# Kernel tuning notes

Measured on AMD Instinct MI355X. Metric: run time of the kernel, lower is better.

Reference implementation:

```python
import jax, jax.numpy as jnp
import numpy as np

N = 50000      # nodes
E = 400000     # edges
IN = 64        # in_channels
HID = 64       # hidden_channels
H = 4          # num_heads
LAT = 32       # latent_dim
NEG_SLOPE = 0.2


def setup_inputs() -> dict:
    key = jax.random.key(0)
    ks = jax.random.split(key, 20)
    w = lambda k, shape, s=0.05: (jax.random.normal(k, shape, jnp.float32) * s)
    inp = {
        'x': jax.random.normal(ks[0], (N, IN), jnp.float32),
        'edge_index': jax.random.randint(ks[1], (2, E), 0, N, dtype=jnp.int32),
        'batch': jnp.zeros((N,), jnp.int32),
        'eps': jax.random.normal(ks[2], (N, LAT), jnp.float32),
        # conv1: in -> HID per head, 4 heads, concat
        'W1': w(ks[3], (IN, H * HID)), 'a_src1': w(ks[4], (H, HID)), 'a_dst1': w(ks[5], (H, HID)), 'b1': jnp.zeros((H * HID,), jnp.float32),
        # conv2: H*HID -> HID per head, concat
        'W2': w(ks[6], (H * HID, H * HID)), 'a_src2': w(ks[7], (H, HID)), 'a_dst2': w(ks[8], (H, HID)), 'b2': jnp.zeros((H * HID,), jnp.float32),
        # conv_mu / conv_logvar: H*HID -> LAT, 1 head, no concat
        'Wmu': w(ks[9], (H * HID, LAT)), 'a_src_mu': w(ks[10], (1, LAT)), 'a_dst_mu': w(ks[11], (1, LAT)), 'b_mu': jnp.zeros((LAT,), jnp.float32),
        'Wlv': w(ks[12], (H * HID, LAT)), 'a_src_lv': w(ks[13], (1, LAT)), 'a_dst_lv': w(ks[14], (1, LAT)), 'b_lv': jnp.zeros((LAT,), jnp.float32),
        # decoder
        'W_fc': w(ks[15], (LAT, HID)), 'b_fc': jnp.zeros((HID,), jnp.float32),
        'W_node': w(ks[16], (HID, IN)), 'b_node': jnp.zeros((IN,), jnp.float32),
        'W_edge': w(ks[17], (HID, 1)), 'b_edge': jnp.zeros((1,), jnp.float32),
    }
    return inp


def gat_layer(x, W, a_src, a_dst, b, src, dst, concat):
    """PyG-style GATConv: gather -> leaky_relu score -> per-dst softmax -> scatter-add."""
    n = x.shape[0]
    heads, c = a_src.shape
    h = (x @ W).reshape(n, heads, c)                     # [N,H,C]
    s_src = jnp.einsum('nhc,hc->nh', h, a_src)           # [N,H]
    s_dst = jnp.einsum('nhc,hc->nh', h, a_dst)
    e = jax.nn.leaky_relu(s_src[src] + s_dst[dst], NEG_SLOPE)   # [E,H]
    m = jax.ops.segment_max(e, dst, num_segments=n)      # stable softmax per destination
    e = jnp.exp(e - m[dst])
    denom = jax.ops.segment_sum(e, dst, num_segments=n)
    alpha = e / (denom[dst] + 1e-16)                     # [E,H]
    out = jax.ops.segment_sum(alpha[:, :, None] * h[src], dst, num_segments=n)  # [N,H,C]
    out = out.reshape(n, heads * c) if concat else out.mean(axis=1)
    return out + b


def reference(x, edge_index, batch, eps,
              W1, a_src1, a_dst1, b1,
              W2, a_src2, a_dst2, b2,
              Wmu, a_src_mu, a_dst_mu, b_mu,
              Wlv, a_src_lv, a_dst_lv, b_lv,
              W_fc, b_fc, W_node, b_node, W_edge, b_edge):
    n = x.shape[0]
    src0, dst0 = edge_index[0], edge_index[1]
    loops = jnp.arange(n, dtype=edge_index.dtype)        # GATConv add_self_loops=True
    src = jnp.concatenate([src0, loops])
    dst = jnp.concatenate([dst0, loops])

    # encode
    h = jax.nn.relu(gat_layer(x, W1, a_src1, a_dst1, b1, src, dst, concat=True))
    h = jax.nn.relu(gat_layer(h, W2, a_src2, a_dst2, b2, src, dst, concat=True))
    mu = gat_layer(h, Wmu, a_src_mu, a_dst_mu, b_mu, src, dst, concat=False)
    logvar = gat_layer(h, Wlv, a_src_lv, a_dst_lv, b_lv, src, dst, concat=False)

    # reparameterize (eps supplied for determinism)
    z = mu + eps * jnp.exp(0.5 * logvar)

    # decode
    zd = jax.nn.relu(z @ W_fc + b_fc)                    # [N,HID]
    node_features = zd @ W_node + b_node                 # [N,IN]
    edge_feat = zd[src0] * zd[dst0]                      # [E,HID]
    edge_scores = (edge_feat @ W_edge + b_edge).squeeze(-1)  # [E]
    return (mu, logvar, z, node_features, edge_scores)
```

## Files before the change

kernel.cpp:

```cpp
#include <hip/hip_runtime.h>
#include <math.h>

#define NEG_SLOPE 0.2f

__device__ __forceinline__ float lky(float x){ return x > 0.f ? x : NEG_SLOPE * x; }

__device__ __forceinline__ unsigned short f2bf(float f){
  unsigned int u = __float_as_uint(f);
  unsigned int r = (u + 0x7fffu + ((u >> 16) & 1u)) >> 16;
  return (unsigned short)r;
}
__device__ __forceinline__ float bf2f(unsigned short s){
  return __uint_as_float(((unsigned int)s) << 16);
}
__device__ __forceinline__ void unp8(uint4 v, float* f){
  f[0]=__uint_as_float(v.x<<16); f[1]=__uint_as_float(v.x&0xffff0000u);
  f[2]=__uint_as_float(v.y<<16); f[3]=__uint_as_float(v.y&0xffff0000u);
  f[4]=__uint_as_float(v.z<<16); f[5]=__uint_as_float(v.z&0xffff0000u);
  f[6]=__uint_as_float(v.w<<16); f[7]=__uint_as_float(v.w&0xffff0000u);
}
__device__ __forceinline__ uint4 pack8(const float* o){
  uint4 v;
  v.x = (unsigned)f2bf(o[0]) | ((unsigned)f2bf(o[1])<<16);
  v.y = (unsigned)f2bf(o[2]) | ((unsigned)f2bf(o[3])<<16);
  v.z = (unsigned)f2bf(o[4]) | ((unsigned)f2bf(o[5])<<16);
  v.w = (unsigned)f2bf(o[6]) | ((unsigned)f2bf(o[7])<<16);
  return v;
}

typedef __bf16 bf16x8 __attribute__((ext_vector_type(8)));
typedef float  f32x4  __attribute__((ext_vector_type(4)));
typedef float  f32x2  __attribute__((ext_vector_type(2)));

__device__ __forceinline__ uint2 pk_fp8(const float* f){
  unsigned lo = 0u, hi = 0u;
  lo = __builtin_amdgcn_cvt_pk_fp8_f32(f[0], f[1], (int)lo, false);
  lo = __builtin_amdgcn_cvt_pk_fp8_f32(f[2], f[3], (int)lo, true);
  hi = __builtin_amdgcn_cvt_pk_fp8_f32(f[4], f[5], (int)hi, false);
  hi = __builtin_amdgcn_cvt_pk_fp8_f32(f[6], f[7], (int)hi, true);
  return make_uint2(lo, hi);
}
__device__ __forceinline__ void unpk_fp8(uint2 v, float* f){
  f32x2 a0 = __builtin_amdgcn_cvt_pk_f32_fp8((int)v.x, false);
  f32x2 a1 = __builtin_amdgcn_cvt_pk_f32_fp8((int)v.x, true);
  f32x2 a2 = __builtin_amdgcn_cvt_pk_f32_fp8((int)v.y, false);
  f32x2 a3 = __builtin_amdgcn_cvt_pk_f32_fp8((int)v.y, true);
  f[0]=a0[0]; f[1]=a0[1]; f[2]=a1[0]; f[3]=a1[1];
  f[4]=a2[0]; f[5]=a2[1]; f[6]=a3[0]; f[7]=a3[1];
}

__global__ void zero_ints_kernel(int* __restrict__ p, int n){
  int i = blockIdx.x * blockDim.x + threadIdx.x;
  if (i < n) p[i] = 0;
}
__global__ void count_deg_kernel(const int* __restrict__ dst, int* __restrict__ deg, int E){
  int e = blockIdx.x * blockDim.x + threadIdx.x;
  if (e < E) atomicAdd(&deg[dst[e]], 1);
}
__global__ void scan_chunk_kernel(const int* __restrict__ deg, int* __restrict__ rowptr,
                                  int* __restrict__ bsum, int n){
  __shared__ int s[256];
  int t = threadIdx.x;
  int i = blockIdx.x * 256 + t;
  int v = (i < n) ? deg[i] : 0;
  s[t] = v; __syncthreads();
  for (int off = 1; off < 256; off <<= 1){
    int x = (t >= off) ? s[t - off] : 0;
    __syncthreads();
    s[t] += x;
    __syncthreads();
  }
  if (i < n) rowptr[i + 1] = s[t];
  if (t == 255) bsum[blockIdx.x] = s[255];
}
__global__ void scan_bsum_kernel(const int* __restrict__ bsum, int* __restrict__ boff, int nb){
  __shared__ int s[256];
  int t = threadIdx.x;
  int v = (t < nb) ? bsum[t] : 0;
  s[t] = v; __syncthreads();
  for (int off = 1; off < 256; off <<= 1){
    int x = (t >= off) ? s[t - off] : 0;
    __syncthreads();
    s[t] += x;
    __syncthreads();
  }
  boff[t] = s[t] - v;
}
__global__ void scan_add_kernel(int* __restrict__ rowptr, const int* __restrict__ boff, int n){
  int i = blockIdx.x * 256 + threadIdx.x;
  if (i < n) rowptr[i + 1] += boff[blockIdx.x];
  if (i == 0) rowptr[0] = 0;
}
__global__ void fill_csr_kernel(const int* __restrict__ src, const int* __restrict__ dst,
                                const int* __restrict__ rowptr, int* __restrict__ cursor,
                                int* __restrict__ colv, int E){
  int e = blockIdx.x * blockDim.x + threadIdx.x;
  if (e >= E) return;
  int d = dst[e];
  int pos = atomicAdd(&cursor[d], 1);
  colv[rowptr[d] + pos] = src[e];
}

__global__ void pack_w_kernel(const float* __restrict__ Wa, const float* __restrict__ Wb,
                              int K, int M, int Mhalf, unsigned short* __restrict__ out){
  int idx = blockIdx.x * 256 + threadIdx.x;
  if (idx >= K * M) return;
  int j = idx & 7;
  int l = (idx >> 3) & 63;
  int rest = idx >> 9;
  int KS = K >> 5;
  int s = rest % KS, gct = rest / KS;
  int col = gct * 16 + (l & 15);
  int k   = s * 32 + ((l >> 4) << 3) + j;
  float v;
  if (Wb == nullptr) v = Wa[(long)k * M + col];
  else v = (col < Mhalf) ? Wa[(long)k * Mhalf + col] : Wb[(long)k * Mhalf + (col - Mhalf)];
  out[idx] = f2bf(v);
}

__global__ void make_p1_kernel(const float* __restrict__ W1, const float* __restrict__ as1,
                               const float* __restrict__ ad1, float* __restrict__ P1){
  int idx = blockIdx.x * 256 + threadIdx.x;
  if (idx >= 512) return;
  int sd = idx & 1, h = (idx >> 1) & 3, k = idx >> 3;
  const float* av = sd ? ad1 : as1;
  float acc = 0.f;
  for (int c = 0; c < 64; ++c) acc += W1[k * 256 + h * 64 + c] * av[h * 64 + c];
  P1[idx] = acc;
}

__global__ __launch_bounds__(256) void score1cvt_kernel(
    const float* __restrict__ x, const float* __restrict__ P1,
    unsigned short* __restrict__ xb,
    float* __restrict__ S1s, float* __restrict__ S1d, int n)
{
  __shared__ float P[512];
  int t = threadIdx.x;
  P[t] = P1[t]; P[t + 256] = P1[t + 256];
  __syncthreads();
  int nid = blockIdx.x * 256 + t;
  if (nid >= n) return;
  const float4* xr = (const float4*)x + (long)nid * 16;
  uint4* xw = (uint4*)xb + (long)nid * 8;
  float acc[8] = {0,0,0,0,0,0,0,0};
  for (int kc = 0; kc < 16; kc += 2){
    float4 v0 = xr[kc], v1 = xr[kc + 1];
    uint4 o;
    o.x = (unsigned)f2bf(v0.x) | ((unsigned)f2bf(v0.y) << 16);
    o.y = (unsigned)f2bf(v0.z) | ((unsigned)f2bf(v0.w) << 16);
    o.z = (unsigned)f2bf(v1.x) | ((unsigned)f2bf(v1.y) << 16);
    o.w = (unsigned)f2bf(v1.z) | ((unsigned)f2bf(v1.w) << 16);
    xw[kc >> 1] = o;
    float vf[8] = {v0.x, v0.y, v0.z, v0.w, v1.x, v1.y, v1.z, v1.w};
    #pragma unroll
    for (int j = 0; j < 8; ++j){
      int k = kc * 4 + j;
      #pragma unroll
      for (int o8 = 0; o8 < 8; ++o8) acc[o8] += vf[j] * P[k * 8 + o8];
    }
  }
  *(float4*)(S1s + nid * 4) = make_float4(acc[0], acc[2], acc[4], acc[6]);
  *(float4*)(S1d + nid * 4) = make_float4(acc[1], acc[3], acc[5], acc[7]);
}

__global__ __launch_bounds__(256) void aggx_kernel(
    const unsigned short* __restrict__ xb,
    const float* __restrict__ Ss, const float* __restrict__ Sd,
    const int* __restrict__ rowptr, const int* __restrict__ colv,
    unsigned short* __restrict__ Xagg, int n)
{
  int wv = threadIdx.x >> 6, l = threadIdx.x & 63;
  int nid = blockIdx.x * 4 + wv;
  if (nid >= n) return;
  int slot = l >> 5;
  int cl = l & 31;
  float4 sdv = *(const float4*)(Sd + (long)nid * 4);
  float acc[4][2] = {};
  float sumw[4] = {0.f, 0.f, 0.f, 0.f};
  int beg = rowptr[nid], end = rowptr[nid + 1];
  for (int jj = beg + slot; jj < end; jj += 2){
    int s = colv[jj];
    float4 a = *(const float4*)(Ss + (long)s * 4);
    float wx = __expf(lky(a.x + sdv.x));
    float wy = __expf(lky(a.y + sdv.y));
    float wz = __expf(lky(a.z + sdv.z));
    float ww = __expf(lky(a.w + sdv.w));
    unsigned xv = *((const unsigned*)xb + (long)s * 32 + cl);
    float f0 = __uint_as_float(xv << 16);
    float f1 = __uint_as_float(xv & 0xffff0000u);
    acc[0][0] += wx * f0; acc[0][1] += wx * f1;
    acc[1][0] += wy * f0; acc[1][1] += wy * f1;
    acc[2][0] += wz * f0; acc[2][1] += wz * f1;
    acc[3][0] += ww * f0; acc[3][1] += ww * f1;
    sumw[0] += wx; sumw[1] += wy; sumw[2] += wz; sumw[3] += ww;
  }
  #pragma unroll
  for (int h = 0; h < 4; ++h){
    acc[h][0] += __shfl_xor(acc[h][0], 32);
    acc[h][1] += __shfl_xor(acc[h][1], 32);
    sumw[h]   += __shfl_xor(sumw[h], 32);
  }
  float4 ssv = *(const float4*)(Ss + (long)nid * 4);
  unsigned xv = *((const unsigned*)xb + (long)nid * 32 + cl);
  float f0 = __uint_as_float(xv << 16);
  float f1 = __uint_as_float(xv & 0xffff0000u);
  float wsh[4] = { __expf(lky(ssv.x + sdv.x)), __expf(lky(ssv.y + sdv.y)),
                   __expf(lky(ssv.z + sdv.z)), __expf(lky(ssv.w + sdv.w)) };
  if (l < 32){
    #pragma unroll
    for (int h = 0; h < 4; ++h){
      float inv = 1.f / (sumw[h] + wsh[h] + 1e-16f);
      float o0 = (acc[h][0] + wsh[h] * f0) * inv;
      float o1 = (acc[h][1] + wsh[h] * f1) * inv;
      unsigned ov = (unsigned)f2bf(o0) | ((unsigned)f2bf(o1) << 16);
      *((unsigned*)Xagg + (long)nid * 128 + h * 32 + cl) = ov;
    }
  }
}

template<int K, int KB, int CW, bool BD, bool SCORES, bool RELU, bool OUT8>
__global__ __launch_bounds__(256) void gemm_mfma_kernel(
    const unsigned short* __restrict__ Xb, const unsigned short* __restrict__ Wpk,
    const float* __restrict__ a_s, const float* __restrict__ a_d,
    const float* __restrict__ a_s2, const float* __restrict__ a_d2,
    const float* __restrict__ bias,
    void* __restrict__ Hout,
    float* __restrict__ Ss, float* __restrict__ Sd,
    float* __restrict__ Ss2, float* __restrict__ Sd2, int n)
{
  constexpr int BR  = (CW == 4) ? 32 : 128;
  constexpr int M   = 64 * CW;
  constexpr int KSB = KB / 32;
  constexpr int LDA = K + 8;
  constexpr int SH  = (BR * LDA > BR * M) ? BR * LDA : BR * M;
  __shared__ unsigned short As[SH];

  const int t = threadIdx.x;
  const int w = t >> 6, l = t & 63;
  const int quad = l >> 4, l15 = l & 15;
  const long base = (long)blockIdx.x * BR;
  const int roww = (CW == 4) ? 0 : w;
  const int colw = (CW == 4) ? w : 0;
  const int abase = BD ? w * KB : 0;

  {
    const uint4* Xg = (const uint4*)Xb;
    long g0 = base * (K / 8);
    long lim = (long)n * (K / 8);
    for (int c = t; c < BR * K / 8; c += 256){
      int row = c / (K / 8), kc = c % (K / 8);
      uint4 v = make_uint4(0u, 0u, 0u, 0u);
      if (g0 + c < lim) v = Xg[g0 + c];
      *(uint4*)(As + row * LDA + kc * 8) = v;
    }
  }
  __syncthreads();

  f32x4 acc[2][4] = {};
  for (int s = 0; s < KSB; ++s){
    bf16x8 af0 = *(const bf16x8*)(As + (roww * 32 + 0  + l15) * LDA + abase + s * 32 + quad * 8);
    bf16x8 af1 = *(const bf16x8*)(As + (roww * 32 + 16 + l15) * LDA + abase + s * 32 + quad * 8);
    #pragma unroll
    for (int ct = 0; ct < 4; ++ct){
      int gct = colw * 4 + ct;
      bf16x8 bf = *(const bf16x8*)(Wpk + (((long)gct * KSB + s) * 64 + l) * 8);
      acc[0][ct] = __builtin_amdgcn_mfma_f32_16x16x32_bf16(af0, bf, acc[0][ct], 0, 0, 0);
      acc[1][ct] = __builtin_amdgcn_mfma_f32_16x16x32_bf16(af1, bf, acc[1][ct], 0, 0, 0);
    }
  }

  if constexpr (SCORES){
    if (CW == 4){
      const int head = w;
      float asv[4], adv[4];
      #pragma unroll
      for (int ct = 0; ct < 4; ++ct){
        int col = head * 64 + ct * 16 + l15;
        asv[ct] = a_s[col]; adv[ct] = a_d[col];
      }
      #pragma unroll
      for (int rt = 0; rt < 2; ++rt){
        #pragma unroll
        for (int r = 0; r < 4; ++r){
          float ps = 0.f, pd = 0.f;
          #pragma unroll
          for (int ct = 0; ct < 4; ++ct){
            float v = acc[rt][ct][r];
            ps += v * asv[ct]; pd += v * adv[ct];
          }
          ps += __shfl_xor(ps, 8); pd += __shfl_xor(pd, 8);
          ps += __shfl_xor(ps, 4); pd += __shfl_xor(pd, 4);
          ps += __shfl_xor(ps, 2); pd += __shfl_xor(pd, 2);
          ps += __shfl_xor(ps, 1); pd += __shfl_xor(pd, 1);
          long node = base + rt * 16 + quad * 4 + r;
          if (l15 == 0 && node < n){ Ss[node * 4 + head] = ps; Sd[node * 4 + head] = pd; }
        }
      }
    } else {
      float asm_[2], adm_[2], asl_[2], adl_[2];
      #pragma unroll
      for (int ct = 0; ct < 2; ++ct){
        int col = ct * 16 + l15;
        asm_[ct] = a_s[col];  adm_[ct] = a_d[col];
        asl_[ct] = a_s2[col]; adl_[ct] = a_d2[col];
      }
      #pragma unroll
      for (int rt = 0; rt < 2; ++rt){
        #pragma unroll
        for (int r = 0; r < 4; ++r){
          float psm = 0.f, pdm = 0.f, psl = 0.f, pdl = 0.f;
          #pragma unroll
          for (int ct = 0; ct < 2; ++ct){
            float vm = acc[rt][ct][r];
            float vl = acc[rt][ct + 2][r];
            psm += vm * asm_[ct]; pdm += vm * adm_[ct];
            psl += vl * asl_[ct]; pdl += vl * adl_[ct];
          }
          #pragma unroll
          for (int d = 8; d >= 1; d >>= 1){
            psm += __shfl_xor(psm, d); pdm += __shfl_xor(pdm, d);
            psl += __shfl_xor(psl, d); pdl += __shfl_xor(pdl, d);
          }
          long node = base + w * 32 + rt * 16 + quad * 4 + r;
          if (l15 == 0 && node < n){
            Ss[node]  = psm; Sd[node]  = pdm;
            Ss2[node] = psl; Sd2[node] = pdl;
          }
        }
      }
    }
  }

  __syncthreads();
  float bct[4] = {0.f, 0.f, 0.f, 0.f};
  if constexpr (RELU){
    #pragma unroll
    for (int ct = 0; ct < 4; ++ct) bct[ct] = bias[colw * 64 + ct * 16 + l15];
  }
  #pragma unroll
  for (int rt = 0; rt < 2; ++rt){
    #pragma unroll
    for (int ct = 0; ct < 4; ++ct){
      #pragma unroll
      for (int r = 0; r < 4; ++r){
        int row = roww * 32 + rt * 16 + quad * 4 + r;
        int col = colw * 64 + ct * 16 + l15;
        float o = acc[rt][ct][r];
        if constexpr (RELU) o = fmaxf(o + bct[ct], 0.f);
        As[row * M + col] = f2bf(o);
      }
    }
  }
  __syncthreads();
  if constexpr (OUT8){
    uint2* Hg = (uint2*)Hout;
    for (int c = t; c < BR * M / 8; c += 256){
      int row = c / (M / 8);
      uint4 v = *(const uint4*)(As + c * 8);
      float f[8]; unp8(v, f);
      if (base + row < n) Hg[base * (M / 8) + c] = pk_fp8(f);
    }
  } else {
    uint4* Hg = (uint4*)Hout;
    for (int c = t; c < BR * M / 8; c += 256){
      int row = c / (M / 8);
      if (base + row < n) Hg[base * (M / 8) + c] = *(const uint4*)(As + c * 8);
    }
  }
}

__global__ __launch_bounds__(256) void agg256_kernel(
    const unsigned char* __restrict__ H8,
    const float* __restrict__ Ss, const float* __restrict__ Sd,
    const int* __restrict__ rowptr, const int* __restrict__ colv,
    const float* __restrict__ bias, unsigned short* __restrict__ Out, int n)
{
  int wv = threadIdx.x >> 6, l = threadIdx.x & 63;
  int nid = blockIdx.x * 4 + wv;
  if (nid >= n) return;
  int slot = l >> 5;
  int cl = l & 31;
  int head = cl >> 3;
  float sdv = Sd[(long)nid * 4 + head];
  const uint2* H8v = (const uint2*)H8;
  float acc[8] = {0,0,0,0,0,0,0,0};
  float sumw = 0.f;
  int beg = rowptr[nid], end = rowptr[nid + 1];
  for (int jj = beg + slot; jj < end; jj += 2){
    int s = colv[jj];
    float wt = __expf(lky(Ss[(long)s * 4 + head] + sdv));
    uint2 hv = H8v[(long)s * 32 + cl];
    float xf[8]; unpk_fp8(hv, xf);
    #pragma unroll
    for (int j = 0; j < 8; ++j) acc[j] += wt * xf[j];
    sumw += wt;
  }
  #pragma unroll
  for (int j = 0; j < 8; ++j) acc[j] += __shfl_xor(acc[j], 32);
  sumw += __shfl_xor(sumw, 32);
  float wself = __expf(lky(Ss[(long)nid * 4 + head] + sdv));
  uint2 hv = H8v[(long)nid * 32 + cl];
  float xf[8]; unpk_fp8(hv, xf);
  if (l < 32){
    float inv = 1.f / (sumw + wself + 1e-16f);
    float4 bv0 = *(const float4*)(bias + cl * 8);
    float4 bv1 = *(const float4*)(bias + cl * 8 + 4);
    float o[8];
    o[0] = fmaxf((acc[0] + wself * xf[0]) * inv + bv0.x, 0.f);
    o[1] = fmaxf((acc[1] + wself * xf[1]) * inv + bv0.y, 0.f);
    o[2] = fmaxf((acc[2] + wself * xf[2]) * inv + bv0.z, 0.f);
    o[3] = fmaxf((acc[3] + wself * xf[3]) * inv + bv0.w, 0.f);
    o[4] = fmaxf((acc[4] + wself * xf[4]) * inv + bv1.x, 0.f);
    o[5] = fmaxf((acc[5] + wself * xf[5]) * inv + bv1.y, 0.f);
    o[6] = fmaxf((acc[6] + wself * xf[6]) * inv + bv1.z, 0.f);
    o[7] = fmaxf((acc[7] + wself * xf[7]) * inv + bv1.w, 0.f);
    *((uint4*)Out + (long)nid * 32 + cl) = pack8(o);
  }
}

__global__ __launch_bounds__(256) void agg_muv_kernel(
    const unsigned short* __restrict__ Hmuv,
    const float* __restrict__ Ssm, const float* __restrict__ Sdm,
    const float* __restrict__ Ssl, const float* __restrict__ Sdl,
    const int* __restrict__ rowptr, const int* __restrict__ colv,
    const float* __restrict__ bmu, const float* __restrict__ blv,
    const float* __restrict__ epsv,
    float* __restrict__ out_mu, float* __restrict__ out_lv, float* __restrict__ out_z,
    unsigned short* __restrict__ zb, int n)
{
  int gid = blockIdx.x * blockDim.x + threadIdx.x;
  int node = gid >> 5, c = gid & 31;
  if (node >= n) return;
  float sdm = Sdm[node], sdl = Sdl[node];
  float wm = __expf(lky(Ssm[node] + sdm));
  float wl = __expf(lky(Ssl[node] + sdl));
  float summ = wm, suml = wl;
  float am = wm * bf2f(Hmuv[(long)node * 64 + c]);
  float al = wl * bf2f(Hmuv[(long)node * 64 + 32 + c]);
  int beg = rowptr[node], end = rowptr[node + 1];
  for (int jj = beg; jj < end; ++jj){
    int s = colv[jj];
    float w1 = __expf(lky(Ssm[s] + sdm));
    float w2 = __expf(lky(Ssl[s] + sdl));
    summ += w1; am += w1 * bf2f(Hmuv[(long)s * 64 + c]);
    suml += w2; al += w2 * bf2f(Hmuv[(long)s * 64 + 32 + c]);
  }
  float mu = am / (summ + 1e-16f) + bmu[c];
  float lv = al / (suml + 1e-16f) + blv[c];
  float z  = mu + epsv[(long)node * 32 + c] * expf(0.5f * lv);
  out_mu[(long)node * 32 + c] = mu;
  out_lv[(long)node * 32 + c] = lv;
  out_z [(long)node * 32 + c] = z;
  zb[(long)node * 32 + c] = f2bf(z);
}

__global__ __launch_bounds__(256) void decoder_mfma_kernel(
    const unsigned short* __restrict__ zb,
    const unsigned short* __restrict__ Wfcpk, const float* __restrict__ bfc,
    const unsigned short* __restrict__ Wndpk, const float* __restrict__ bnode,
    unsigned short* __restrict__ ZD, float* __restrict__ NF, int n)
{
  constexpr int LDA = 40;
  constexpr int LDZ = 72;
  __shared__ unsigned short As[128 * LDA];
  __shared__ unsigned short Zs[128 * LDZ];
  const int t = threadIdx.x;
  const int w = t >> 6, l = t & 63;
  const int quad = l >> 4, l15 = l & 15;
  const long base = (long)blockIdx.x * 128;

  {
    const uint4* Zg = (const uint4*)zb;
    long g0 = base * 4;
    long lim = (long)n * 4;
    for (int c = t; c < 512; c += 256){
      int row = c >> 2, kc = c & 3;
      uint4 v = make_uint4(0u, 0u, 0u, 0u);
      if (g0 + c < lim) v = Zg[g0 + c];
      *(uint4*)(As + row * LDA + kc * 8) = v;
    }
  }
  __syncthreads();

  f32x4 acc[2][4] = {};
  {
    bf16x8 af0 = *(const bf16x8*)(As + (w * 32 + 0  + l15) * LDA + quad * 8);
    bf16x8 af1 = *(const bf16x8*)(As + (w * 32 + 16 + l15) * LDA + quad * 8);
    #pragma unroll
    for (int ct = 0; ct < 4; ++ct){
      bf16x8 bf = *(const bf16x8*)(Wfcpk + (((long)ct) * 64 + l) * 8);
      acc[0][ct] = __builtin_amdgcn_mfma_f32_16x16x32_bf16(af0, bf, acc[0][ct], 0, 0, 0);
      acc[1][ct] = __builtin_amdgcn_mfma_f32_16x16x32_bf16(af1, bf, acc[1][ct], 0, 0, 0);
    }
  }
  #pragma unroll
  for (int rt = 0; rt < 2; ++rt){
    #pragma unroll
    for (int ct = 0; ct < 4; ++ct){
      float b = bfc[ct * 16 + l15];
      #pragma unroll
      for (int r = 0; r < 4; ++r){
        int row = w * 32 + rt * 16 + quad * 4 + r;
        Zs[row * LDZ + ct * 16 + l15] = f2bf(fmaxf(acc[rt][ct][r] + b, 0.f));
      }
    }
  }
  __syncthreads();

  {
    uint4* Zgo = (uint4*)ZD;
    for (int c = t; c < 1024; c += 256){
      int row = c >> 3, kc = c & 7;
      if (base + row < n) Zgo[base * 8 + c] = *(const uint4*)(Zs + row * LDZ + kc * 8);
    }
  }

  f32x4 acc2[2][4] = {};
  #pragma unroll
  for (int s = 0; s < 2; ++s){
    bf16x8 af0 = *(const bf16x8*)(Zs + (w * 32 + 0  + l15) * LDZ + s * 32 + quad * 8);
    bf16x8 af1 = *(const bf16x8*)(Zs + (w * 32 + 16 + l15) * LDZ + s * 32 + quad * 8);
    #pragma unroll
    for (int ct = 0; ct < 4; ++ct){
      bf16x8 bf = *(const bf16x8*)(Wndpk + (((long)ct * 2 + s) * 64 + l) * 8);
      acc2[0][ct] = __builtin_amdgcn_mfma_f32_16x16x32_bf16(af0, bf, acc2[0][ct], 0, 0, 0);
      acc2[1][ct] = __builtin_amdgcn_mfma_f32_16x16x32_bf16(af1, bf, acc2[1][ct], 0, 0, 0);
    }
  }
  #pragma unroll
  for (int rt = 0; rt < 2; ++rt){
    #pragma unroll
    for (int ct = 0; ct < 4; ++ct){
      float b = bnode[ct * 16 + l15];
      #pragma unroll
      for (int r = 0; r < 4; ++r){
        long row = base + w * 32 + rt * 16 + quad * 4 + r;
        if (row < n) NF[row * 64 + ct * 16 + l15] = acc2[rt][ct][r] + b;
      }
    }
  }
}

__global__ __launch_bounds__(256) void edge_score_kernel(
    const unsigned short* __restrict__ ZD, const int* __restrict__ src, const int* __restrict__ dst,
    const float* __restrict__ Wedge, const float* __restrict__ bedge,
    float* __restrict__ out_es, int E)
{
  int gid = blockIdx.x * 256 + threadIdx.x;
  int l = threadIdx.x & 63;
  int slot = l >> 3, chunk = l & 7;
  int e = (gid >> 6) * 8 + slot;
  float4 we0 = *(const float4*)(Wedge + chunk * 8);
  float4 we1 = *(const float4*)(Wedge + chunk * 8 + 4);
  float p = 0.f;
  if (e < E){
    int s = src[e], d = dst[e];
    uint4 zs_ = *((const uint4*)ZD + (long)s * 8 + chunk);
    uint4 zd_ = *((const uint4*)ZD + (long)d * 8 + chunk);
    float a[8], b[8]; unp8(zs_, a); unp8(zd_, b);
    p = a[0]*b[0]*we0.x + a[1]*b[1]*we0.y + a[2]*b[2]*we0.z + a[3]*b[3]*we0.w
      + a[4]*b[4]*we1.x + a[5]*b[5]*we1.y + a[6]*b[6]*we1.z + a[7]*b[7]*we1.w;
  }
  p += __shfl_xor(p, 1);
  p += __shfl_xor(p, 2);
  p += __shfl_xor(p, 4);
  if (chunk == 0 && e < E) out_es[e] = p + bedge[0];
}

extern "C" void kernel_launch(void* const* d_in, const int* in_sizes, int n_in,
                              void* d_out, int out_size, void* d_ws, size_t ws_size,
                              hipStream_t stream)
{
  const float* x     = (const float*)d_in[0];
  const int*   ei    = (const int*)  d_in[1];
  const float* epsv  = (const float*)d_in[3];
  const float* W1    = (const float*)d_in[4];
  const float* as1   = (const float*)d_in[5];
  const float* ad1   = (const float*)d_in[6];
  const float* b1    = (const float*)d_in[7];
  const float* W2    = (const float*)d_in[8];
  const float* as2   = (const float*)d_in[9];
  const float* ad2   = (const float*)d_in[10];
  const float* b2    = (const float*)d_in[11];
  const float* Wmu   = (const float*)d_in[12];
  const float* asmu  = (const float*)d_in[13];
  const float* admu  = (const float*)d_in[14];
  const float* bmu   = (const float*)d_in[15];
  const float* Wlv   = (const float*)d_in[16];
  const float* aslv  = (const float*)d_in[17];
  const float* adlv  = (const float*)d_in[18];
  const float* blv   = (const float*)d_in[19];
  const float* Wfc   = (const float*)d_in[20];
  const float* bfc   = (const float*)d_in[21];
  const float* Wnode = (const float*)d_in[22];
  const float* bnode = (const float*)d_in[23];
  const float* Wedge = (const float*)d_in[24];
  const float* bedge = (const float*)d_in[25];

  const int N = in_sizes[0] / 64;
  const int E = in_sizes[1] / 2;
  const int* srcA = ei;
  const int* dstA = ei + E;

  char* wsb = (char*)d_ws;
  size_t off = 0;
  auto alloc = [&](size_t bytes) -> void* {
    void* p = wsb + off;
    off += (bytes + 255) & ~(size_t)255;
    return p;
  };
  unsigned short* xb    = (unsigned short*)alloc((size_t)N * 64 * 2);
  unsigned short* bufP  = (unsigned short*)alloc((size_t)N * 256 * 2);
  unsigned short* bufQ  = (unsigned short*)alloc((size_t)N * 256 * 2);
  unsigned char*  H8    = (unsigned char*) alloc((size_t)N * 256);
  unsigned short* Hmuv  = (unsigned short*)alloc((size_t)N * 64 * 2);
  unsigned short* ZDb   = (unsigned short*)alloc((size_t)N * 64 * 2);
  unsigned short* zbb   = (unsigned short*)alloc((size_t)N * 32 * 2);
  unsigned short* W1pk  = (unsigned short*)alloc((size_t)64 * 256 * 2);
  unsigned short* W2pk  = (unsigned short*)alloc((size_t)256 * 256 * 2);
  unsigned short* Wmvpk = (unsigned short*)alloc((size_t)256 * 64 * 2);
  unsigned short* Wfcpk = (unsigned short*)alloc((size_t)32 * 64 * 2);
  unsigned short* Wndpk = (unsigned short*)alloc((size_t)64 * 64 * 2);
  float* P1    = (float*)alloc(512 * 4);
  float* S1s   = (float*)alloc((size_t)N * 4 * 4);
  float* S1d   = (float*)alloc((size_t)N * 4 * 4);
  float* S2s   = (float*)alloc((size_t)N * 4 * 4);
  float* S2d   = (float*)alloc((size_t)N * 4 * 4);
  float* Ssm   = (float*)alloc((size_t)N * 4);
  float* Sdm   = (float*)alloc((size_t)N * 4);
  float* Ssl   = (float*)alloc((size_t)N * 4);
  float* Sdl   = (float*)alloc((size_t)N * 4);
  int*   deg   = (int*)  alloc((size_t)N * 2 * 4);
  int*   cursor= deg + N;
  int*   rowptr= (int*)  alloc((size_t)(N + 1) * 4);
  int*   colv  = (int*)  alloc((size_t)E * 4);
  int*   bsum  = (int*)  alloc(1024);
  int*   boff  = (int*)  alloc(1024);
  (void)ws_size; (void)n_in; (void)out_size;

  float* out_mu = (float*)d_out;
  float* out_lv = out_mu + (size_t)N * 32;
  float* out_z  = out_lv + (size_t)N * 32;
  float* out_nf = out_z  + (size_t)N * 32;
  float* out_es = out_nf + (size_t)N * 64;

  const int nb = (N + 255) / 256;

  zero_ints_kernel<<<(2 * N + 255) / 256, 256, 0, stream>>>(deg, 2 * N);
  count_deg_kernel<<<(E + 255) / 256, 256, 0, stream>>>(dstA, deg, E);
  scan_chunk_kernel<<<nb, 256, 0, stream>>>(deg, rowptr, bsum, N);
  scan_bsum_kernel<<<1, 256, 0, stream>>>(bsum, boff, nb);
  scan_add_kernel<<<nb, 256, 0, stream>>>(rowptr, boff, N);
  fill_csr_kernel<<<(E + 255) / 256, 256, 0, stream>>>(srcA, dstA, rowptr, cursor, colv, E);

  pack_w_kernel<<<(64 * 256 + 255) / 256, 256, 0, stream>>>(W1, nullptr, 64, 256, 256, W1pk);
  pack_w_kernel<<<(256 * 256 + 255) / 256, 256, 0, stream>>>(W2, nullptr, 256, 256, 256, W2pk);
  pack_w_kernel<<<(256 * 64 + 255) / 256, 256, 0, stream>>>(Wmu, Wlv, 256, 64, 32, Wmvpk);
  pack_w_kernel<<<(32 * 64 + 255) / 256, 256, 0, stream>>>(Wfc, nullptr, 32, 64, 64, Wfcpk);
  pack_w_kernel<<<(64 * 64 + 255) / 256, 256, 0, stream>>>(Wnode, nullptr, 64, 64, 64, Wndpk);
  make_p1_kernel<<<2, 256, 0, stream>>>(W1, as1, ad1, P1);

  score1cvt_kernel<<<(N + 255) / 256, 256, 0, stream>>>(x, P1, xb, S1s, S1d, N);
  aggx_kernel<<<(N + 3) / 4, 256, 0, stream>>>(xb, S1s, S1d, rowptr, colv, bufP, N);
  gemm_mfma_kernel<256, 64, 4, true, false, true, false><<<(N + 31) / 32, 256, 0, stream>>>(
      bufP, W1pk, nullptr, nullptr, nullptr, nullptr, b1, bufQ,
      nullptr, nullptr, nullptr, nullptr, N);

  gemm_mfma_kernel<256, 256, 4, false, true, false, true><<<(N + 31) / 32, 256, 0, stream>>>(
      bufQ, W2pk, as2, ad2, nullptr, nullptr, nullptr, H8,
      S2s, S2d, nullptr, nullptr, N);
  agg256_kernel<<<(N + 3) / 4, 256, 0, stream>>>(H8, S2s, S2d, rowptr, colv, b2, bufP, N);

  gemm_mfma_kernel<256, 256, 1, false, true, false, false><<<(N + 127) / 128, 256, 0, stream>>>(
      bufP, Wmvpk, asmu, admu, aslv, adlv, nullptr, Hmuv,
      Ssm, Sdm, Ssl, Sdl, N);
  agg_muv_kernel<<<((size_t)N * 32 + 255) / 256, 256, 0, stream>>>(
      Hmuv, Ssm, Sdm, Ssl, Sdl, rowptr, colv, bmu, blv, epsv,
      out_mu, out_lv, out_z, zbb, N);

  decoder_mfma_kernel<<<(N + 127) / 128, 256, 0, stream>>>(
      zbb, Wfcpk, bfc, Wndpk, bnode, ZDb, out_nf, N);
  {
    long waves = ((long)E + 7) / 8;
    long blocks = (waves + 3) / 4;
    edge_score_kernel<<<(int)blocks, 256, 0, stream>>>(ZDb, srcA, dstA, Wedge, bedge, out_es, E);
  }
}
```

Measured before the change: 365.5 us.

## Fuse setup kernels, interleave mu/logvar, restructure mu/lv aggregation, store decoder output fp8

Several launches are merged: the two scan-offset kernels become one, and the five weight-pack kernels plus the P1 precompute become a single kernel. The mu/logvar GEMM now interleaves the two heads so one 32-bit load yields both. The mu/lv aggregation moves to one wave per node, with two edge slots reduced by shuffle. The decoder's ZD intermediate is stored as fp8 instead of bf16, halving the gather bytes in the edge-score kernel at some cost in precision.

```diff
diff --git a/kernel.cpp b/kernel.cpp
--- a/kernel.cpp
+++ b/kernel.cpp
@@ -39,6 +39,12 @@
   hi = __builtin_amdgcn_cvt_pk_fp8_f32(f[4], f[5], (int)hi, false);
   hi = __builtin_amdgcn_cvt_pk_fp8_f32(f[6], f[7], (int)hi, true);
   return make_uint2(lo, hi);
+}
+__device__ __forceinline__ unsigned pk_fp8x4(float f0, float f1, float f2, float f3){
+  unsigned u = 0u;
+  u = __builtin_amdgcn_cvt_pk_fp8_f32(f0, f1, (int)u, false);
+  u = __builtin_amdgcn_cvt_pk_fp8_f32(f2, f3, (int)u, true);
+  return u;
 }
 __device__ __forceinline__ void unpk_fp8(uint2 v, float* f){
   f32x2 a0 = __builtin_amdgcn_cvt_pk_f32_fp8((int)v.x, false);
@@ -73,7 +79,8 @@
   if (i < n) rowptr[i + 1] = s[t];
   if (t == 255) bsum[blockIdx.x] = s[255];
 }
-__global__ void scan_bsum_kernel(const int* __restrict__ bsum, int* __restrict__ boff, int nb){
+__global__ void scan_add_kernel(int* __restrict__ rowptr, const int* __restrict__ bsum,
+                                int nb, int n){
   __shared__ int s[256];
   int t = threadIdx.x;
   int v = (t < nb) ? bsum[t] : 0;
@@ -84,11 +91,10 @@
     s[t] += x;
     __syncthreads();
   }
-  boff[t] = s[t] - v;
-}
-__global__ void scan_add_kernel(int* __restrict__ rowptr, const int* __restrict__ boff, int n){
-  int i = blockIdx.x * 256 + threadIdx.x;
-  if (i < n) rowptr[i + 1] += boff[blockIdx.x];
+  int b = blockIdx.x;
+  int excl = (b == 0) ? 0 : s[b - 1];
+  int i = b * 256 + t;
+  if (i < n) rowptr[i + 1] += excl;
   if (i == 0) rowptr[0] = 0;
 }
 __global__ void fill_csr_kernel(const int* __restrict__ src, const int* __restrict__ dst,
@@ -101,9 +107,9 @@
   colv[rowptr[d] + pos] = src[e];
 }
 
-__global__ void pack_w_kernel(const float* __restrict__ Wa, const float* __restrict__ Wb,
-                              int K, int M, int Mhalf, unsigned short* __restrict__ out){
-  int idx = blockIdx.x * 256 + threadIdx.x;
+__device__ __forceinline__ void pack_one(const float* Wa, const float* Wb,
+                                         int K, int M, int Mhalf,
+                                         unsigned short* out, int idx){
   if (idx >= K * M) return;
   int j = idx & 7;
   int l = (idx >> 3) & 63;
@@ -118,15 +124,37 @@
   out[idx] = f2bf(v);
 }
 
-__global__ void make_p1_kernel(const float* __restrict__ W1, const float* __restrict__ as1,
-                               const float* __restrict__ ad1, float* __restrict__ P1){
-  int idx = blockIdx.x * 256 + threadIdx.x;
-  if (idx >= 512) return;
-  int sd = idx & 1, h = (idx >> 1) & 3, k = idx >> 3;
-  const float* av = sd ? ad1 : as1;
-  float acc = 0.f;
-  for (int c = 0; c < 64; ++c) acc += W1[k * 256 + h * 64 + c] * av[h * 64 + c];
-  P1[idx] = acc;
+__global__ __launch_bounds__(256) void packall_kernel(
+    const float* __restrict__ W1,  unsigned short* __restrict__ W1pk,
+    const float* __restrict__ W2,  unsigned short* __restrict__ W2pk,
+    const float* __restrict__ Wmu, const float* __restrict__ Wlv,
+    unsigned short* __restrict__ Wmvpk,
+    const float* __restrict__ Wfc, unsigned short* __restrict__ Wfcpk,
+    const float* __restrict__ Wnd, unsigned short* __restrict__ Wndpk,
+    const float* __restrict__ as1, const float* __restrict__ ad1,
+    float* __restrict__ P1)
+{
+  int b = blockIdx.x, t = threadIdx.x;
+  if (b < 64){
+    pack_one(W1, nullptr, 64, 256, 256, W1pk, b * 256 + t);
+  } else if (b < 320){
+    pack_one(W2, nullptr, 256, 256, 256, W2pk, (b - 64) * 256 + t);
+  } else if (b < 384){
+    pack_one(Wmu, Wlv, 256, 64, 32, Wmvpk, (b - 320) * 256 + t);
+  } else if (b < 392){
+    pack_one(Wfc, nullptr, 32, 64, 64, Wfcpk, (b - 384) * 256 + t);
+  } else if (b < 408){
+    pack_one(Wnd, nullptr, 64, 64, 64, Wndpk, (b - 392) * 256 + t);
+  } else {
+    int idx = (b - 408) * 256 + t;
+    if (idx < 512){
+      int sd = idx & 1, h = (idx >> 1) & 3, k = idx >> 3;
+      const float* av = sd ? ad1 : as1;
+      float acc = 0.f;
+      for (int c = 0; c < 64; ++c) acc += W1[k * 256 + h * 64 + c] * av[h * 64 + c];
+      P1[idx] = acc;
+    }
+  }
 }
 
 __global__ __launch_bounds__(256) void score1cvt_kernel(
@@ -347,7 +375,9 @@
         int col = colw * 64 + ct * 16 + l15;
         float o = acc[rt][ct][r];
         if constexpr (RELU) o = fmaxf(o + bct[ct], 0.f);
-        As[row * M + col] = f2bf(o);
+        int pos = col;
+        if constexpr (CW == 1){ pos = (col < 32) ? (col * 2) : ((col - 32) * 2 + 1); }
+        As[row * M + pos] = f2bf(o);
       }
     }
   }
@@ -428,37 +458,48 @@
     float* __restrict__ out_mu, float* __restrict__ out_lv, float* __restrict__ out_z,
     unsigned short* __restrict__ zb, int n)
 {
-  int gid = blockIdx.x * blockDim.x + threadIdx.x;
-  int node = gid >> 5, c = gid & 31;
-  if (node >= n) return;
-  float sdm = Sdm[node], sdl = Sdl[node];
-  float wm = __expf(lky(Ssm[node] + sdm));
-  float wl = __expf(lky(Ssl[node] + sdl));
-  float summ = wm, suml = wl;
-  float am = wm * bf2f(Hmuv[(long)node * 64 + c]);
-  float al = wl * bf2f(Hmuv[(long)node * 64 + 32 + c]);
-  int beg = rowptr[node], end = rowptr[node + 1];
-  for (int jj = beg; jj < end; ++jj){
+  int wv = threadIdx.x >> 6, l = threadIdx.x & 63;
+  int nid = blockIdx.x * 4 + wv;
+  if (nid >= n) return;
+  int slot = l >> 5;
+  int cl = l & 31;
+  float sdm = Sdm[nid], sdl = Sdl[nid];
+  const unsigned* Hm32 = (const unsigned*)Hmuv;
+  float am = 0.f, al = 0.f, summ = 0.f, suml = 0.f;
+  int beg = rowptr[nid], end = rowptr[nid + 1];
+  for (int jj = beg + slot; jj < end; jj += 2){
     int s = colv[jj];
-    float w1 = __expf(lky(Ssm[s] + sdm));
-    float w2 = __expf(lky(Ssl[s] + sdl));
-    summ += w1; am += w1 * bf2f(Hmuv[(long)s * 64 + c]);
-    suml += w2; al += w2 * bf2f(Hmuv[(long)s * 64 + 32 + c]);
-  }
-  float mu = am / (summ + 1e-16f) + bmu[c];
-  float lv = al / (suml + 1e-16f) + blv[c];
-  float z  = mu + epsv[(long)node * 32 + c] * expf(0.5f * lv);
-  out_mu[(long)node * 32 + c] = mu;
-  out_lv[(long)node * 32 + c] = lv;
-  out_z [(long)node * 32 + c] = z;
-  zb[(long)node * 32 + c] = f2bf(z);
+    float wm = __expf(lky(Ssm[s] + sdm));
+    float wl = __expf(lky(Ssl[s] + sdl));
+    unsigned hv = Hm32[(long)s * 32 + cl];
+    float mu = __uint_as_float(hv << 16);
+    float lv = __uint_as_float(hv & 0xffff0000u);
+    am += wm * mu; al += wl * lv;
+    summ += wm; suml += wl;
+  }
+  am += __shfl_xor(am, 32); al += __shfl_xor(al, 32);
+  summ += __shfl_xor(summ, 32); suml += __shfl_xor(suml, 32);
+  float wms = __expf(lky(Ssm[nid] + sdm));
+  float wls = __expf(lky(Ssl[nid] + sdl));
+  unsigned hv = Hm32[(long)nid * 32 + cl];
+  float mus = __uint_as_float(hv << 16);
+  float lvs = __uint_as_float(hv & 0xffff0000u);
+  if (l < 32){
+    float mu = (am + wms * mus) / (summ + wms + 1e-16f) + bmu[cl];
+    float lv = (al + wls * lvs) / (suml + wls + 1e-16f) + blv[cl];
+    float z  = mu + epsv[(long)nid * 32 + cl] * expf(0.5f * lv);
+    out_mu[(long)nid * 32 + cl] = mu;
+    out_lv[(long)nid * 32 + cl] = lv;
+    out_z [(long)nid * 32 + cl] = z;
+    zb[(long)nid * 32 + cl] = f2bf(z);
+  }
 }
 
 __global__ __launch_bounds__(256) void decoder_mfma_kernel(
     const unsigned short* __restrict__ zb,
     const unsigned short* __restrict__ Wfcpk, const float* __restrict__ bfc,
     const unsigned short* __restrict__ Wndpk, const float* __restrict__ bnode,
-    unsigned short* __restrict__ ZD, float* __restrict__ NF, int n)
+    unsigned char* __restrict__ ZD8, float* __restrict__ NF, int n)
 {
   constexpr int LDA = 40;
   constexpr int LDZ = 72;
@@ -508,10 +549,15 @@
   __syncthreads();
 
   {
-    uint4* Zgo = (uint4*)ZD;
-    for (int c = t; c < 1024; c += 256){
-      int row = c >> 3, kc = c & 7;
-      if (base + row < n) Zgo[base * 8 + c] = *(const uint4*)(Zs + row * LDZ + kc * 8);
+    unsigned* Zgo = (unsigned*)ZD8;
+    for (int c = t; c < 2048; c += 256){
+      int row = c >> 4, kc = c & 15;
+      uint2 v = *(const uint2*)(Zs + row * LDZ + kc * 4);
+      float f0 = __uint_as_float(v.x << 16);
+      float f1 = __uint_as_float(v.x & 0xffff0000u);
+      float f2 = __uint_as_float(v.y << 16);
+      float f3 = __uint_as_float(v.y & 0xffff0000u);
+      if (base + row < n) Zgo[base * 16 + c] = pk_fp8x4(f0, f1, f2, f3);
     }
   }
 
@@ -542,7 +588,7 @@
 }
 
 __global__ __launch_bounds__(256) void edge_score_kernel(
-    const unsigned short* __restrict__ ZD, const int* __restrict__ src, const int* __restrict__ dst,
+    const unsigned char* __restrict__ ZD8, const int* __restrict__ src, const int* __restrict__ dst,
     const float* __restrict__ Wedge, const float* __restrict__ bedge,
     float* __restrict__ out_es, int E)
 {
@@ -555,9 +601,9 @@
   float p = 0.f;
   if (e < E){
     int s = src[e], d = dst[e];
-    uint4 zs_ = *((const uint4*)ZD + (long)s * 8 + chunk);
-    uint4 zd_ = *((const uint4*)ZD + (long)d * 8 + chunk);
-    float a[8], b[8]; unp8(zs_, a); unp8(zd_, b);
+    uint2 zs_ = *((const uint2*)ZD8 + (long)s * 8 + chunk);
+    uint2 zd_ = *((const uint2*)ZD8 + (long)d * 8 + chunk);
+    float a[8], b[8]; unpk_fp8(zs_, a); unpk_fp8(zd_, b);
     p = a[0]*b[0]*we0.x + a[1]*b[1]*we0.y + a[2]*b[2]*we0.z + a[3]*b[3]*we0.w
       + a[4]*b[4]*we1.x + a[5]*b[5]*we1.y + a[6]*b[6]*we1.z + a[7]*b[7]*we1.w;
   }
@@ -614,7 +660,7 @@
   unsigned short* bufQ  = (unsigned short*)alloc((size_t)N * 256 * 2);
   unsigned char*  H8    = (unsigned char*) alloc((size_t)N * 256);
   unsigned short* Hmuv  = (unsigned short*)alloc((size_t)N * 64 * 2);
-  unsigned short* ZDb   = (unsigned short*)alloc((size_t)N * 64 * 2);
+  unsigned char*  ZD8   = (unsigned char*) alloc((size_t)N * 64);
   unsigned short* zbb   = (unsigned short*)alloc((size_t)N * 32 * 2);
   unsigned short* W1pk  = (unsigned short*)alloc((size_t)64 * 256 * 2);
   unsigned short* W2pk  = (unsigned short*)alloc((size_t)256 * 256 * 2);
@@ -635,7 +681,6 @@
   int*   rowptr= (int*)  alloc((size_t)(N + 1) * 4);
   int*   colv  = (int*)  alloc((size_t)E * 4);
   int*   bsum  = (int*)  alloc(1024);
-  int*   boff  = (int*)  alloc(1024);
   (void)ws_size; (void)n_in; (void)out_size;
 
   float* out_mu = (float*)d_out;
@@ -649,16 +694,11 @@
   zero_ints_kernel<<<(2 * N + 255) / 256, 256, 0, stream>>>(deg, 2 * N);
   count_deg_kernel<<<(E + 255) / 256, 256, 0, stream>>>(dstA, deg, E);
   scan_chunk_kernel<<<nb, 256, 0, stream>>>(deg, rowptr, bsum, N);
-  scan_bsum_kernel<<<1, 256, 0, stream>>>(bsum, boff, nb);
-  scan_add_kernel<<<nb, 256, 0, stream>>>(rowptr, boff, N);
+  scan_add_kernel<<<nb, 256, 0, stream>>>(rowptr, bsum, nb, N);
   fill_csr_kernel<<<(E + 255) / 256, 256, 0, stream>>>(srcA, dstA, rowptr, cursor, colv, E);
 
-  pack_w_kernel<<<(64 * 256 + 255) / 256, 256, 0, stream>>>(W1, nullptr, 64, 256, 256, W1pk);
-  pack_w_kernel<<<(256 * 256 + 255) / 256, 256, 0, stream>>>(W2, nullptr, 256, 256, 256, W2pk);
-  pack_w_kernel<<<(256 * 64 + 255) / 256, 256, 0, stream>>>(Wmu, Wlv, 256, 64, 32, Wmvpk);
-  pack_w_kernel<<<(32 * 64 + 255) / 256, 256, 0, stream>>>(Wfc, nullptr, 32, 64, 64, Wfcpk);
-  pack_w_kernel<<<(64 * 64 + 255) / 256, 256, 0, stream>>>(Wnode, nullptr, 64, 64, 64, Wndpk);
-  make_p1_kernel<<<2, 256, 0, stream>>>(W1, as1, ad1, P1);
+  packall_kernel<<<410, 256, 0, stream>>>(W1, W1pk, W2, W2pk, Wmu, Wlv, Wmvpk,
+                                          Wfc, Wfcpk, Wnode, Wndpk, as1, ad1, P1);
 
   score1cvt_kernel<<<(N + 255) / 256, 256, 0, stream>>>(x, P1, xb, S1s, S1d, N);
   aggx_kernel<<<(N + 3) / 4, 256, 0, stream>>>(xb, S1s, S1d, rowptr, colv, bufP, N);
@@ -674,15 +714,15 @@
   gemm_mfma_kernel<256, 256, 1, false, true, false, false><<<(N + 127) / 128, 256, 0, stream>>>(
       bufP, Wmvpk, asmu, admu, aslv, adlv, nullptr, Hmuv,
       Ssm, Sdm, Ssl, Sdl, N);
-  agg_muv_kernel<<<((size_t)N * 32 + 255) / 256, 256, 0, stream>>>(
+  agg_muv_kernel<<<(N + 3) / 4, 256, 0, stream>>>(
       Hmuv, Ssm, Sdm, Ssl, Sdl, rowptr, colv, bmu, blv, epsv,
       out_mu, out_lv, out_z, zbb, N);
 
   decoder_mfma_kernel<<<(N + 127) / 128, 256, 0, stream>>>(
-      zbb, Wfcpk, bfc, Wndpk, bnode, ZDb, out_nf, N);
+      zbb, Wfcpk, bfc, Wndpk, bnode, ZD8, out_nf, N);
   {
     long waves = ((long)E + 7) / 8;
     long blocks = (waves + 3) / 4;
-    edge_score_kernel<<<(int)blocks, 256, 0, stream>>>(ZDb, srcA, dstA, Wedge, bedge, out_es, E);
-  }
-}
+    edge_score_kernel<<<(int)blocks, 256, 0, stream>>>(ZD8, srcA, dstA, Wedge, bedge, out_es, E);
+  }
+}
```

Result: faster. 354.3 us (-3.1%).
